# Kernel tuning notes

Measured on AMD Instinct MI355X. Metric: run time of the kernel, lower is better.

Reference implementation:

```python
import jax, jax.numpy as jnp
import numpy as np

NUM_TOKEN = 1024
IN_DIM = 512
OUT_DIM = 512
E = 1024          # expansion_factor * in_token_dims
S = 128
EPS = 1e-5
SQRT_S = float(np.sqrt(S))


def _rope_seq(x):
    """RoPE over axis 1 (sequence), last axis is feature dim. x: [B, L, ..., D]."""
    L = x.shape[1]
    half = x.shape[-1] // 2
    pos = jnp.arange(L, dtype=jnp.float32)
    inv_freq = 10000.0 ** (jnp.arange(half, dtype=jnp.float32) / half)
    sinusoid = pos[:, None] * inv_freq[None, :]          # [L, half]
    bshape = (1, L) + (1,) * (x.ndim - 3) + (half,)
    sin = jnp.sin(sinusoid).reshape(bshape)
    cos = jnp.cos(sinusoid).reshape(bshape)
    x1, x2 = jnp.split(x, 2, axis=-1)
    return jnp.concatenate([x1 * cos - x2 * sin, x2 * cos + x1 * sin], axis=-1)


def setup_inputs() -> dict:
    key = jax.random.key(0)
    ks = jax.random.split(key, 8)
    B = 32
    x = jax.random.normal(ks[0], (B, NUM_TOKEN, IN_DIM), jnp.float32)
    uv_w = jax.random.normal(ks[1], (2 * E + S, IN_DIM), jnp.float32) / np.sqrt(IN_DIM)
    o_w = jax.random.normal(ks[2], (OUT_DIM, E), jnp.float32) / np.sqrt(E)
    gamma = jax.random.uniform(ks[3], (2, S), jnp.float32)
    beta = jax.random.uniform(ks[4], (2, S), jnp.float32)
    w = jax.random.uniform(ks[5], (2 * NUM_TOKEN - 1,), jnp.float32)
    g = jnp.ones((1,), jnp.float32)                       # ScaleNorm gain
    res_scale = jnp.ones((IN_DIM,), jnp.float32)
    layer_scale = jnp.ones((OUT_DIM,), jnp.float32)
    return dict(x=x, uv_w=uv_w, o_w=o_w, gamma=gamma, beta=beta, w=w,
                g=g, res_scale=res_scale, layer_scale=layer_scale)


def reference(x, uv_w, o_w, gamma, beta, w, g, res_scale, layer_scale):
    B, L, D = x.shape
    # ScaleNorm
    norm = jnp.linalg.norm(x, axis=-1, keepdims=True) * (D ** -0.5)
    xn = x / jnp.maximum(norm, EPS) * g
    # shift mixing (time shift: first half channels shifted right by 1 token)
    xs, xp = jnp.split(xn, 2, axis=-1)
    xs = jnp.pad(xs, ((0, 0), (1, 0), (0, 0)))[:, :L, :]
    xn = jnp.concatenate([xs, xp], axis=-1)
    # uv projection + SiLU, then split into u, v, base
    uv = jax.nn.silu(xn @ uv_w.T)                         # [B, L, 2E+S]
    u, v, base = jnp.split(uv, [E, 2 * E], axis=-1)
    # per-head affine then RoPE
    base = base[:, :, None, :] * gamma[None, None] + beta  # [B, L, 2, S]
    base = _rope_seq(base)
    q, k = base[:, :, 0, :], base[:, :, 1, :]
    qk = jnp.einsum('bls,bms->blm', q, k)                 # [B, L, L]
    # structure-mode relative position bias: bias[i, j] = w[j - i + L - 1]
    idx = jnp.arange(L)[None, :] - jnp.arange(L)[:, None] + (L - 1)
    qk = qk + w[idx][None]
    kernel = jnp.square(jax.nn.relu(qk / SQRT_S))
    out = u * jnp.einsum('blm,bme->ble', kernel, v)       # gated quadratic attn
    out = out @ o_w.T                                     # [B, L, OUT_DIM]
    return x * res_scale + out * layer_scale
```

## Files before the change

### kernel.cpp

```cpp
#include <hip/hip_runtime.h>
#include <hip/hip_bf16.h>
#include <math.h>

typedef unsigned short u16;
typedef __bf16 bf16x8 __attribute__((ext_vector_type(8)));
typedef float f32x4 __attribute__((ext_vector_type(4)));

#define NB 32
#define LSEQ 1024
#define DIN 512
#define EDIM 1024
#define SDIM 128
#define NTOK (NB * LSEQ)
#define NUV 2176
#define CHUNK 16

#define AS1 __attribute__((address_space(1)))
#define AS3 __attribute__((address_space(3)))

__device__ __forceinline__ u16 f2bf(float f) {
  unsigned u = __builtin_bit_cast(unsigned, f);
  u += 0x7fffu + ((u >> 16) & 1u);
  return (u16)(u >> 16);
}
__device__ __forceinline__ float bf2f(u16 h) {
  unsigned u = ((unsigned)h) << 16;
  return __builtin_bit_cast(float, u);
}
__device__ __forceinline__ float fast_silu(float x) {
  float t = __builtin_amdgcn_exp2f(-1.44269504088896f * x);
  return x * __builtin_amdgcn_rcpf(1.0f + t);
}


__global__ __launch_bounds__(256) void k_f32_to_bf16(const float* __restrict__ in,
                                                     u16* __restrict__ out, int n4) {
  int i = blockIdx.x * 256 + threadIdx.x;
  if (i < n4) {
    float4 f = ((const float4*)in)[i];
    ushort4 o;
    o.x = f2bf(f.x); o.y = f2bf(f.y); o.z = f2bf(f.z); o.w = f2bf(f.w);
    ((ushort4*)out)[i] = o;
  }
}

__global__ __launch_bounds__(256) void k_normshift(const float* __restrict__ x,
                                                   const float* __restrict__ g,
                                                   u16* __restrict__ xn2) {
  int t = blockIdx.x;
  int l = t & (LSEQ - 1);
  float2 v = ((const float2*)(x + (size_t)t * DIN))[threadIdx.x];
  float ss = v.x * v.x + v.y * v.y;
  for (int o = 32; o > 0; o >>= 1) ss += __shfl_down(ss, o, 64);
  __shared__ float p[4];
  if ((threadIdx.x & 63) == 0) p[threadIdx.x >> 6] = ss;
  __syncthreads();
  float s = p[0] + p[1] + p[2] + p[3];
  float norm = sqrtf(s * (1.0f / (float)DIN));
  float inv = g[0] / fmaxf(norm, 1e-5f);
  int d = threadIdx.x * 2;
  ushort2 ob; ob.x = f2bf(v.x * inv); ob.y = f2bf(v.y * inv);
  if (d >= 256) {
    *(ushort2*)(xn2 + (size_t)t * DIN + d) = ob;
  } else {
    if (l < LSEQ - 1) *(ushort2*)(xn2 + (size_t)(t + 1) * DIN + d) = ob;
    if (l == 0) { ushort2 z = {0, 0}; *(ushort2*)(xn2 + (size_t)t * DIN + d) = z; }
  }
}

__global__ __launch_bounds__(256) void k_rope_table(float* __restrict__ sin_t,
                                                    float* __restrict__ cos_t) {
  int idx = blockIdx.x * 256 + threadIdx.x;
  int l = idx >> 6, j = idx & 63;
  double freq = pow(10000.0, (double)j / 64.0);
  float arg = (float)l * (float)freq;
  double a = (double)arg;
  sin_t[idx] = (float)sin(a);
  cos_t[idx] = (float)cos(a);
}

__global__ __launch_bounds__(256) void k_qkbuild(const u16* __restrict__ base,
                                                 const float* __restrict__ gamma,
                                                 const float* __restrict__ beta,
                                                 const float* __restrict__ sin_t,
                                                 const float* __restrict__ cos_t,
                                                 u16* __restrict__ q, u16* __restrict__ k) {
  int idx = blockIdx.x * 256 + threadIdx.x;
  int t = idx >> 6, j = idx & 63;
  int l = t & (LSEQ - 1);
  float b1 = bf2f(base[(size_t)t * SDIM + j]);
  float b2 = bf2f(base[(size_t)t * SDIM + j + 64]);
  float s = sin_t[l * 64 + j], c = cos_t[l * 64 + j];
  {
    float y1 = b1 * gamma[j] + beta[j];
    float y2 = b2 * gamma[64 + j] + beta[64 + j];
    q[(size_t)t * SDIM + j]      = f2bf(y1 * c - y2 * s);
    q[(size_t)t * SDIM + j + 64] = f2bf(y2 * c + y1 * s);
  }
  {
    float y1 = b1 * gamma[128 + j] + beta[128 + j];
    float y2 = b2 * gamma[192 + j] + beta[192 + j];
    k[(size_t)t * SDIM + j]      = f2bf(y1 * c - y2 * s);
    k[(size_t)t * SDIM + j + 64] = f2bf(y2 * c + y1 * s);
  }
}


__device__ __forceinline__ void stage128x32(const u16* g, int ld, u16* l, int tid) {
  int r = tid >> 2;
  int c = ((tid & 3) ^ ((tid >> 3) & 3)) * 8;
  const u16* g0 = g + (size_t)r * ld + c;
  const u16* g1 = g + (size_t)(r + 64) * ld + c;
  u16* l0 = l + tid * 8;
  u16* l1 = l + tid * 8 + 2048;
  __builtin_amdgcn_global_load_lds((AS1 unsigned int*)g0, (AS3 unsigned int*)l0, 16, 0, 0);
  __builtin_amdgcn_global_load_lds((AS1 unsigned int*)g1, (AS3 unsigned int*)l1, 16, 0, 0);
}

__device__ __forceinline__ void gemm_core(const u16* A, const u16* B, int K,
                                          int lda, int ldb,
                                          u16* sA, u16* sB, f32x4 acc[4][4]) {
  const int tid = threadIdx.x;
  const int lane = tid & 63;
  const int wid = tid >> 6;
  const int wr = wid >> 1, wc = wid & 1;
  const int fr = lane & 15, kg = lane >> 4;
  const int ks = (kg ^ ((fr >> 1) & 3)) * 8;
  const u16* sa_base = sA + (wr * 64 + fr) * 32 + ks;
  const u16* sb_base = sB + (wc * 64 + fr) * 32 + ks;
  for (int k0 = 0; k0 < K; k0 += 32) {
    stage128x32(A + k0, lda, sA, tid);
    stage128x32(B + k0, ldb, sB, tid);
    __syncthreads();
    bf16x8 a[4], b[4];
#pragma unroll
    for (int i = 0; i < 4; ++i) a[i] = *(const bf16x8*)(sa_base + i * 16 * 32);
#pragma unroll
    for (int i = 0; i < 4; ++i) b[i] = *(const bf16x8*)(sb_base + i * 16 * 32);
#pragma unroll
    for (int m = 0; m < 4; ++m)
#pragma unroll
      for (int n = 0; n < 4; ++n)
        acc[m][n] = __builtin_amdgcn_mfma_f32_16x16x32_bf16(a[m], b[n], acc[m][n], 0, 0, 0);
    __syncthreads();
  }
}


__device__ __forceinline__ void stage256x64(const u16* __restrict__ g, int ld,
                                            u16* __restrict__ lds, int tid) {
#pragma unroll
  for (int j = 0; j < 4; ++j) {
    int idx = tid + j * 512;
    int row = idx >> 3;
    int sc = ((idx & 7) ^ (row & 7)) * 8;
    const u16* src = g + (size_t)row * ld + sc;
    __builtin_amdgcn_global_load_lds((AS1 unsigned int*)src,
                                     (AS3 unsigned int*)(lds + idx * 8), 16, 0, 0);
  }
}

__device__ __forceinline__ void gemm256_core(const u16* A, int lda,
                                             const u16* B, int ldb,
                                             int K, u16* smem, f32x4 (&acc)[8][4]) {
  const int tid = threadIdx.x;
  const int lane = tid & 63, wid = tid >> 6;
  const int wr = wid >> 2, wc = wid & 3;
  const int fr = lane & 15, kg = lane >> 4;
  u16* A0 = smem;
  u16* B0 = smem + 16384;
  u16* A1 = smem + 32768;
  u16* B1 = smem + 49152;
  const int nt = K >> 6;
  stage256x64(A, lda, A0, tid);
  stage256x64(B, ldb, B0, tid);
  stage256x64(A + 64, lda, A1, tid);
  stage256x64(B + 64, ldb, B1, tid);
  asm volatile("s_waitcnt vmcnt(8)" ::: "memory");
  __builtin_amdgcn_sched_barrier(0);
  __builtin_amdgcn_s_barrier();
  for (int t = 0; t < nt; ++t) {
    u16* cA = (t & 1) ? A1 : A0;
    u16* cB = (t & 1) ? B1 : B0;
    bf16x8 b[4][2];
#pragma unroll
    for (int q = 0; q < 4; ++q) {
      bf16x8 a[2][2];
#pragma unroll
      for (int r = 0; r < 2; ++r)
#pragma unroll
        for (int h = 0; h < 2; ++h) {
          int row = wr * 128 + (q * 2 + r) * 16 + fr;
          int slot = (h * 4 + kg) ^ (fr & 7);
          a[r][h] = *(const bf16x8*)(cA + row * 64 + slot * 8);
        }
      if (q == 0) {
#pragma unroll
        for (int n = 0; n < 4; ++n)
#pragma unroll
          for (int h = 0; h < 2; ++h) {
            int row = wc * 64 + n * 16 + fr;
            int slot = (h * 4 + kg) ^ (fr & 7);
            b[n][h] = *(const bf16x8*)(cB + row * 64 + slot * 8);
          }
      }
      __builtin_amdgcn_s_barrier();
      __builtin_amdgcn_s_setprio(1);
#pragma unroll
      for (int r = 0; r < 2; ++r)
#pragma unroll
        for (int n = 0; n < 4; ++n)
#pragma unroll
          for (int h = 0; h < 2; ++h)
            acc[q * 2 + r][n] = __builtin_amdgcn_mfma_f32_16x16x32_bf16(
                a[r][h], b[n][h], acc[q * 2 + r][n], 0, 0, 0);
      __builtin_amdgcn_s_setprio(0);
      __builtin_amdgcn_s_barrier();
    }
    if (t + 2 < nt) {
      stage256x64(A + (size_t)(t + 2) * 64, lda, cA, tid);
      stage256x64(B + (size_t)(t + 2) * 64, ldb, cB, tid);
      asm volatile("s_waitcnt vmcnt(8)" ::: "memory");
    } else {
      asm volatile("s_waitcnt vmcnt(0)" ::: "memory");
    }
    __builtin_amdgcn_sched_barrier(0);
    __builtin_amdgcn_s_barrier();
  }
}

__global__ __launch_bounds__(512, 2) void k_gemm_uv(const u16* __restrict__ xn2,
                                                    const u16* __restrict__ wbf,
                                                    u16* __restrict__ u, u16* __restrict__ vt,
                                                    u16* __restrict__ base) {
  __shared__ __align__(16) u16 smem[65536];
  f32x4 acc[8][4] = {};
  int bid = blockIdx.x;
  int xcd = bid & 7;
  int off = bid >> 3;
  int m0 = (xcd * 16 + off / 9) * 256;
  int n0 = (off % 9) * 256;
  gemm256_core(xn2 + (size_t)m0 * DIN, DIN, wbf + (size_t)n0 * DIN, DIN, DIN, smem, acc);
  int lane = threadIdx.x & 63, wid = threadIdx.x >> 6;
  int wr = wid >> 2, wc = wid & 3;
  int cb = n0 + wc * 64 + (lane & 15);
  int rb = m0 + wr * 128 + (lane >> 4) * 4;
  if (n0 < EDIM) {
#pragma unroll
    for (int mm = 0; mm < 8; ++mm)
#pragma unroll
      for (int n = 0; n < 4; ++n) {
        int c = cb + n * 16;
#pragma unroll
        for (int j = 0; j < 4; ++j) {
          int r = rb + mm * 16 + j;
          u[(size_t)r * EDIM + c] = f2bf(fast_silu(acc[mm][n][j]));
        }
      }
  } else if (n0 < 2 * EDIM) {
    int b = m0 >> 10;
    u16* vtb = vt + (size_t)b * (EDIM * LSEQ);
#pragma unroll
    for (int mm = 0; mm < 8; ++mm) {
      int l0 = (rb + mm * 16) & (LSEQ - 1);
#pragma unroll
      for (int n = 0; n < 4; ++n) {
        int e = cb + n * 16 - EDIM;
        ushort4 o;
        o.x = f2bf(fast_silu(acc[mm][n][0]));
        o.y = f2bf(fast_silu(acc[mm][n][1]));
        o.z = f2bf(fast_silu(acc[mm][n][2]));
        o.w = f2bf(fast_silu(acc[mm][n][3]));
        *(ushort4*)(vtb + (size_t)e * LSEQ + l0) = o;
      }
    }
  } else if (wc < 2) {
#pragma unroll
    for (int mm = 0; mm < 8; ++mm)
#pragma unroll
      for (int n = 0; n < 4; ++n) {
        int c = cb + n * 16 - 2 * EDIM;
#pragma unroll
        for (int j = 0; j < 4; ++j) {
          int r = rb + mm * 16 + j;
          base[(size_t)r * SDIM + c] = f2bf(fast_silu(acc[mm][n][j]));
        }
      }
  }
}

__global__ __launch_bounds__(256) void k_gemm_qk(const u16* __restrict__ q,
                                                 const u16* __restrict__ k,
                                                 const float* __restrict__ w,
                                                 u16* __restrict__ scores) {
  __shared__ __align__(16) u16 sA[4096];
  __shared__ __align__(16) u16 sB[4096];
  f32x4 acc[4][4] = {};
  int bid = blockIdx.x;
  int xcd = bid & 7;
  int off = bid >> 3;
  int b = xcd * 2 + (off >> 6);
  int t = off & 63;
  int m0 = (t >> 3) * 128, n0 = (t & 7) * 128;
  gemm_core(q + (size_t)(b * LSEQ + m0) * SDIM, k + (size_t)(b * LSEQ + n0) * SDIM,
            SDIM, SDIM, SDIM, sA, sB, acc);
  int lane = threadIdx.x & 63, wid = threadIdx.x >> 6;
  int wr = wid >> 1, wc = wid & 1;
  int cb = n0 + wc * 64 + (lane & 15);
  int rb = m0 + wr * 64 + (lane >> 4) * 4;
  const float inv_sqrt_s = 0.08838834764831845f;
  u16* sc_b = scores + (size_t)b * LSEQ * LSEQ;
#pragma unroll
  for (int m = 0; m < 4; ++m)
#pragma unroll
    for (int n = 0; n < 4; ++n) {
      int c = cb + n * 16;
#pragma unroll
      for (int j = 0; j < 4; ++j) {
        int r = rb + m * 16 + j;
        float val = (acc[m][n][j] + w[c - r + (LSEQ - 1)]) * inv_sqrt_s;
        val = fmaxf(val, 0.0f);
        sc_b[(size_t)r * LSEQ + c] = f2bf(val * val);
      }
    }
}

__global__ __launch_bounds__(512, 2) void k_gemm_pv(const u16* __restrict__ scores,
                                                    const u16* __restrict__ vt,
                                                    u16* u_io) {
  __shared__ __align__(16) u16 smem[65536];
  f32x4 acc[8][4] = {};
  int bid = blockIdx.x;
  int xcd = bid & 7;
  int off = bid >> 3;
  int b = xcd * 2 + (off >> 4);
  int t = off & 15;
  int m0 = (t >> 2) * 256, n0 = (t & 3) * 256;
  gemm256_core(scores + (size_t)b * LSEQ * LSEQ + (size_t)m0 * LSEQ, LSEQ,
               vt + (size_t)b * LSEQ * EDIM + (size_t)n0 * LSEQ, LSEQ,
               LSEQ, smem, acc);
  int lane = threadIdx.x & 63, wid = threadIdx.x >> 6;
  int wr = wid >> 2, wc = wid & 3;
  int cb = n0 + wc * 64 + (lane & 15);
  int rb = m0 + wr * 128 + (lane >> 4) * 4;
#pragma unroll
  for (int mm = 0; mm < 8; ++mm)
#pragma unroll
    for (int n = 0; n < 4; ++n) {
      int c = cb + n * 16;
#pragma unroll
      for (int j = 0; j < 4; ++j) {
        int r = rb + mm * 16 + j;
        size_t idx = (size_t)(b * LSEQ + r) * EDIM + c;
        u_io[idx] = f2bf(acc[mm][n][j] * bf2f(u_io[idx]));
      }
    }
}

__global__ __launch_bounds__(512, 2) void k_gemm_out(const u16* __restrict__ attn,
                                                     const u16* __restrict__ owbf,
                                                     const float* __restrict__ x,
                                                     const float* __restrict__ res_scale,
                                                     const float* __restrict__ layer_scale,
                                                     float* __restrict__ out) {
  __shared__ __align__(16) u16 smem[65536];
  f32x4 acc[8][4] = {};
  int bid = blockIdx.x;
  int xcd = bid & 7;
  int off = bid >> 3;
  int m0 = (xcd * 16 + (off >> 1)) * 256;
  int n0 = (off & 1) * 256;
  gemm256_core(attn + (size_t)m0 * EDIM, EDIM, owbf + (size_t)n0 * EDIM, EDIM,
               EDIM, smem, acc);
  int lane = threadIdx.x & 63, wid = threadIdx.x >> 6;
  int wr = wid >> 2, wc = wid & 3;
  int cb = n0 + wc * 64 + (lane & 15);
  int rb = m0 + wr * 128 + (lane >> 4) * 4;
#pragma unroll
  for (int mm = 0; mm < 8; ++mm)
#pragma unroll
    for (int n = 0; n < 4; ++n) {
      int c = cb + n * 16;
#pragma unroll
      for (int j = 0; j < 4; ++j) {
        int r = rb + mm * 16 + j;
        out[(size_t)r * DIN + c] =
            x[(size_t)r * DIN + c] * res_scale[c] + acc[mm][n][j] * layer_scale[c];
      }
    }
}


extern "C" void kernel_launch(void* const* d_in, const int* in_sizes, int n_in,
                              void* d_out, int out_size, void* d_ws, size_t ws_size,
                              hipStream_t stream) {
  const float* x          = (const float*)d_in[0];
  const float* uv_w       = (const float*)d_in[1];
  const float* o_w        = (const float*)d_in[2];
  const float* gamma      = (const float*)d_in[3];
  const float* beta       = (const float*)d_in[4];
  const float* w          = (const float*)d_in[5];
  const float* g          = (const float*)d_in[6];
  const float* res_scale  = (const float*)d_in[7];
  const float* layer_scale= (const float*)d_in[8];
  float* out = (float*)d_out;

  char* ws = (char*)d_ws;
  u16* xn2    = (u16*)(ws + 0);
  u16* q      = (u16*)(ws + 0);
  u16* k      = (u16*)(ws + 8388608);
  u16* scores = (u16*)(ws + 16777216);
  u16* base   = (u16*)(ws + 33554432);
  u16* u_io   = (u16*)(ws + 50331648);
  u16* vt     = (u16*)(ws + 117440512);
  u16* uvw_bf = (u16*)(ws + 184549376);
  u16* ow_bf  = (u16*)(ws + 186908672);
  float* sin_t = (float*)(ws + 187957248);
  float* cos_t = (float*)(ws + 188219392);

  k_f32_to_bf16<<<dim3((NUV * DIN / 4 + 255) / 256), 256, 0, stream>>>(uv_w, uvw_bf, NUV * DIN / 4);
  k_f32_to_bf16<<<dim3((DIN * EDIM / 4 + 255) / 256), 256, 0, stream>>>(o_w, ow_bf, DIN * EDIM / 4);
  k_rope_table<<<dim3(LSEQ * 64 / 256), 256, 0, stream>>>(sin_t, cos_t);
  k_normshift<<<dim3(NTOK), 256, 0, stream>>>(x, g, xn2);

  k_gemm_uv<<<dim3(1152), 512, 0, stream>>>(xn2, uvw_bf, u_io, vt, base);

  k_qkbuild<<<dim3(NTOK * 64 / 256), 256, 0, stream>>>(base, gamma, beta, sin_t, cos_t, q, k);

  for (int ch = 0; ch < NB / CHUNK; ++ch) {
    size_t tok0 = (size_t)ch * CHUNK * LSEQ;
    k_gemm_qk<<<dim3(1024), 256, 0, stream>>>(q + tok0 * SDIM, k + tok0 * SDIM, w, scores);
    k_gemm_pv<<<dim3(256), 512, 0, stream>>>(scores, vt + tok0 * EDIM, u_io + tok0 * EDIM);
  }

  k_gemm_out<<<dim3(256), 512, 0, stream>>>(u_io, ow_bf, x, res_scale, layer_scale, out);
}
```

Baseline: 331.9 us.

## Software-pipeline LDS reads and interleave global-to-LDS staging in 256x256 GEMM core

Replaces the 256x256 bf16 GEMM main loop with a pipelined version. It prefetches the next A fragment from LDS while the current MFMA batch runs, and splits the next-next tile's global-to-LDS staging into four slices placed between MFMA phases. Each wave now stages rows tied to its own row band, with a reworked swizzle and no separate per-iteration stage block. The goal is to hide LDS read latency and spread memory issue across the compute, at the cost of more live registers and finer-grained barrier/vmcnt ordering that must stay correct.

```diff
diff --git a/kernel.cpp b/kernel.cpp
--- a/kernel.cpp
+++ b/kernel.cpp
@@ -147,87 +147,101 @@
 }
 
 
-__device__ __forceinline__ void stage256x64(const u16* __restrict__ g, int ld,
-                                            u16* __restrict__ lds, int tid) {
-#pragma unroll
-  for (int j = 0; j < 4; ++j) {
-    int idx = tid + j * 512;
-    int row = idx >> 3;
-    int sc = ((idx & 7) ^ (row & 7)) * 8;
-    const u16* src = g + (size_t)row * ld + sc;
-    __builtin_amdgcn_global_load_lds((AS1 unsigned int*)src,
-                                     (AS3 unsigned int*)(lds + idx * 8), 16, 0, 0);
-  }
-}
-
-__device__ __forceinline__ void gemm256_core(const u16* A, int lda,
-                                             const u16* B, int ldb,
-                                             int K, u16* smem, f32x4 (&acc)[8][4]) {
+#define GROW_A(s) (wr * 128 + (s) * 32 + wc * 8)
+#define GROW_B(s) (wid * 32 + (s) * 8)
+
+#define STG_PAIR(s, At2, Bt2, dA, dB)                                              \
+  do {                                                                             \
+    __builtin_amdgcn_global_load_lds(                                              \
+        (AS1 unsigned int*)((At2) + (size_t)(GROW_A(s) + srow) * lda + scol),      \
+        (AS3 unsigned int*)((dA) + GROW_A(s) * 64), 16, 0, 0);                     \
+    __builtin_amdgcn_global_load_lds(                                              \
+        (AS1 unsigned int*)((Bt2) + (size_t)(GROW_B(s) + srow) * ldb + scol),      \
+        (AS3 unsigned int*)((dB) + GROW_B(s) * 64), 16, 0, 0);                     \
+  } while (0)
+
+#define RD_A(dst, cbuf, q)                                                         \
+  do {                                                                             \
+    _Pragma("unroll") for (int r_ = 0; r_ < 2; ++r_)                               \
+    _Pragma("unroll") for (int h_ = 0; h_ < 2; ++h_)                               \
+      dst[r_][h_] = *(const bf16x8*)((cbuf) + (wr * 128 + (q) * 32 + r_ * 16 + fr) * 64 + \
+                                     (((h_ * 4 + kg) ^ fr7) * 8));                 \
+  } while (0)
+
+#define RD_B(cbuf)                                                                 \
+  do {                                                                             \
+    _Pragma("unroll") for (int n_ = 0; n_ < 4; ++n_)                               \
+    _Pragma("unroll") for (int h_ = 0; h_ < 2; ++h_)                               \
+      breg[n_][h_] = *(const bf16x8*)((cbuf) + (wc * 64 + n_ * 16 + fr) * 64 +     \
+                                      (((h_ * 4 + kg) ^ fr7) * 8));                \
+  } while (0)
+
+#define MFMA16(s, areg)                                                            \
+  do {                                                                             \
+    __builtin_amdgcn_s_setprio(1);                                                 \
+    _Pragma("unroll") for (int r_ = 0; r_ < 2; ++r_)                               \
+    _Pragma("unroll") for (int n_ = 0; n_ < 4; ++n_)                               \
+    _Pragma("unroll") for (int h_ = 0; h_ < 2; ++h_)                               \
+      acc[(s) * 2 + r_][n_] = __builtin_amdgcn_mfma_f32_16x16x32_bf16(             \
+          areg[r_][h_], breg[n_][h_], acc[(s) * 2 + r_][n_], 0, 0, 0);             \
+    __builtin_amdgcn_s_setprio(0);                                                 \
+  } while (0)
+
+#define BAR_FENCE()                                                                \
+  do { __builtin_amdgcn_s_barrier(); asm volatile("" ::: "memory"); } while (0)
+
+__device__ __forceinline__ void gemm256p_core(const u16* __restrict__ A, int lda,
+                                              const u16* __restrict__ B, int ldb,
+                                              int K, u16* smem, f32x4 (&acc)[8][4]) {
   const int tid = threadIdx.x;
   const int lane = tid & 63, wid = tid >> 6;
   const int wr = wid >> 2, wc = wid & 3;
-  const int fr = lane & 15, kg = lane >> 4;
-  u16* A0 = smem;
-  u16* B0 = smem + 16384;
-  u16* A1 = smem + 32768;
-  u16* B1 = smem + 49152;
+  const int fr = lane & 15, kg = lane >> 4, fr7 = fr & 7;
+  const int srow = lane >> 3;
+  const int scol = ((lane & 7) ^ srow) * 8;
+  u16* cA = smem;
+  u16* cB = smem + 16384;
+  u16* nA = smem + 32768;
+  u16* nB = smem + 49152;
   const int nt = K >> 6;
-  stage256x64(A, lda, A0, tid);
-  stage256x64(B, ldb, B0, tid);
-  stage256x64(A + 64, lda, A1, tid);
-  stage256x64(B + 64, ldb, B1, tid);
+
+#pragma unroll
+  for (int s = 0; s < 4; ++s) STG_PAIR(s, A, B, cA, cB);
+#pragma unroll
+  for (int s = 0; s < 4; ++s) STG_PAIR(s, A + 64, B + 64, nA, nB);
   asm volatile("s_waitcnt vmcnt(8)" ::: "memory");
-  __builtin_amdgcn_sched_barrier(0);
-  __builtin_amdgcn_s_barrier();
+  BAR_FENCE();
+
+  bf16x8 breg[4][2], ac[2][2], an[2][2];
+  RD_B(cB);
+  RD_A(ac, cA, 0);
+
   for (int t = 0; t < nt; ++t) {
-    u16* cA = (t & 1) ? A1 : A0;
-    u16* cB = (t & 1) ? B1 : B0;
-    bf16x8 b[4][2];
-#pragma unroll
-    for (int q = 0; q < 4; ++q) {
-      bf16x8 a[2][2];
-#pragma unroll
-      for (int r = 0; r < 2; ++r)
-#pragma unroll
-        for (int h = 0; h < 2; ++h) {
-          int row = wr * 128 + (q * 2 + r) * 16 + fr;
-          int slot = (h * 4 + kg) ^ (fr & 7);
-          a[r][h] = *(const bf16x8*)(cA + row * 64 + slot * 8);
-        }
-      if (q == 0) {
-#pragma unroll
-        for (int n = 0; n < 4; ++n)
-#pragma unroll
-          for (int h = 0; h < 2; ++h) {
-            int row = wc * 64 + n * 16 + fr;
-            int slot = (h * 4 + kg) ^ (fr & 7);
-            b[n][h] = *(const bf16x8*)(cB + row * 64 + slot * 8);
-          }
-      }
-      __builtin_amdgcn_s_barrier();
-      __builtin_amdgcn_s_setprio(1);
-#pragma unroll
-      for (int r = 0; r < 2; ++r)
-#pragma unroll
-        for (int n = 0; n < 4; ++n)
-#pragma unroll
-          for (int h = 0; h < 2; ++h)
-            acc[q * 2 + r][n] = __builtin_amdgcn_mfma_f32_16x16x32_bf16(
-                a[r][h], b[n][h], acc[q * 2 + r][n], 0, 0, 0);
-      __builtin_amdgcn_s_setprio(0);
-      __builtin_amdgcn_s_barrier();
-    }
-    if (t + 2 < nt) {
-      stage256x64(A + (size_t)(t + 2) * 64, lda, cA, tid);
-      stage256x64(B + (size_t)(t + 2) * 64, ldb, cB, tid);
-      asm volatile("s_waitcnt vmcnt(8)" ::: "memory");
-    } else {
-      asm volatile("s_waitcnt vmcnt(0)" ::: "memory");
-    }
-    __builtin_amdgcn_sched_barrier(0);
-    __builtin_amdgcn_s_barrier();
-  }
-}
+    const bool st = (t + 2) < nt;
+    const u16* At2 = A + (size_t)(t + 2) * 64;
+    const u16* Bt2 = B + (size_t)(t + 2) * 64;
+    MFMA16(0, ac);
+    RD_A(an, cA, 1);
+    BAR_FENCE();
+    if (st) STG_PAIR(0, At2, Bt2, cA, cB);
+    MFMA16(1, an);
+    RD_A(ac, cA, 2);
+    BAR_FENCE();
+    if (st) STG_PAIR(1, At2, Bt2, cA, cB);
+    MFMA16(2, ac);
+    RD_A(an, cA, 3);
+    BAR_FENCE();
+    if (st) STG_PAIR(2, At2, Bt2, cA, cB);
+    MFMA16(3, an);
+    if (st) asm volatile("s_waitcnt vmcnt(6)" ::: "memory");
+    else    asm volatile("s_waitcnt vmcnt(0)" ::: "memory");
+    BAR_FENCE();
+    if (st) STG_PAIR(3, At2, Bt2, cA, cB);
+    { u16* tp = cA; cA = nA; nA = tp; tp = cB; cB = nB; nB = tp; }
+    if (t + 1 < nt) { RD_B(cB); RD_A(ac, cA, 0); }
+  }
+}
+
 
 __global__ __launch_bounds__(512, 2) void k_gemm_uv(const u16* __restrict__ xn2,
                                                     const u16* __restrict__ wbf,
@@ -240,7 +254,7 @@
   int off = bid >> 3;
   int m0 = (xcd * 16 + off / 9) * 256;
   int n0 = (off % 9) * 256;
-  gemm256_core(xn2 + (size_t)m0 * DIN, DIN, wbf + (size_t)n0 * DIN, DIN, DIN, smem, acc);
+  gemm256p_core(xn2 + (size_t)m0 * DIN, DIN, wbf + (size_t)n0 * DIN, DIN, DIN, smem, acc);
   int lane = threadIdx.x & 63, wid = threadIdx.x >> 6;
   int wr = wid >> 2, wc = wid & 3;
   int cb = n0 + wc * 64 + (lane & 15);
@@ -336,9 +350,9 @@
   int b = xcd * 2 + (off >> 4);
   int t = off & 15;
   int m0 = (t >> 2) * 256, n0 = (t & 3) * 256;
-  gemm256_core(scores + (size_t)b * LSEQ * LSEQ + (size_t)m0 * LSEQ, LSEQ,
-               vt + (size_t)b * LSEQ * EDIM + (size_t)n0 * LSEQ, LSEQ,
-               LSEQ, smem, acc);
+  gemm256p_core(scores + (size_t)b * LSEQ * LSEQ + (size_t)m0 * LSEQ, LSEQ,
+                vt + (size_t)b * LSEQ * EDIM + (size_t)n0 * LSEQ, LSEQ,
+                LSEQ, smem, acc);
   int lane = threadIdx.x & 63, wid = threadIdx.x >> 6;
   int wr = wid >> 2, wc = wid & 3;
   int cb = n0 + wc * 64 + (lane & 15);
@@ -370,8 +384,8 @@
   int off = bid >> 3;
   int m0 = (xcd * 16 + (off >> 1)) * 256;
   int n0 = (off & 1) * 256;
-  gemm256_core(attn + (size_t)m0 * EDIM, EDIM, owbf + (size_t)n0 * EDIM, EDIM,
-               EDIM, smem, acc);
+  gemm256p_core(attn + (size_t)m0 * EDIM, EDIM, owbf + (size_t)n0 * EDIM, EDIM,
+                EDIM, smem, acc);
   int lane = threadIdx.x & 63, wid = threadIdx.x >> 6;
   int wr = wid >> 2, wc = wid & 3;
   int cb = n0 + wc * 64 + (lane & 15);
```

Result: faster. 318.5 us (-4.0%).
